# Optimization experiments

Measured on AMD Instinct MI355X. Metric: run time of the kernel, lower is better.

## Reference

```python
import jax, jax.numpy as jnp
import numpy as np

B, S, DM = 4, 8192, 1024
N_RED = 16384   # tokens merged into their right neighbor
N_SAVE = 16384  # tokens kept; must be divisible by B


def setup_inputs() -> dict:
    key = jax.random.key(0)
    k1, k2, k3, k4 = jax.random.split(key, 4)
    x = jax.random.normal(k1, (B, S, DM), dtype=jnp.float32)
    W = jax.random.normal(k2, (DM, DM), dtype=jnp.float32) * (1.0 / np.sqrt(DM))
    ids_to_reduce = jax.random.randint(k3, (N_RED,), 0, B * S - 1, dtype=jnp.int64)
    ids_to_save = jax.random.randint(k4, (N_SAVE,), 0, B * S, dtype=jnp.int64)
    return {"x": x, "W": W, "ids_to_save": ids_to_save, "ids_to_reduce": ids_to_reduce}


def reference(x, W, ids_to_save, ids_to_reduce):
    batch_size, _, dm = x.shape
    xf = x.reshape(-1, dm)                       # [B*S, dm]
    reduced = xf[ids_to_reduce]                  # gather  [N_RED, dm]
    transformed = (reduced @ W.T).astype(jnp.float32)  # Linear, no bias
    xf = xf.at[ids_to_reduce + 1].add(transformed)     # scatter-add into right neighbor
    saved = xf[ids_to_save]                      # gather  [N_SAVE, dm]
    return saved.reshape(batch_size, -1, dm)     # [B, N_SAVE//B, dm]
```

## Files before the change

kernel.cpp:

```cpp
#include <hip/hip_runtime.h>

#define DM    1024
#define NTOK  32768
#define NRED  16384
#define NSAVE 16384

typedef __attribute__((ext_vector_type(8))) short bf16x8;
typedef __attribute__((ext_vector_type(4))) float f32x4;

__device__ __forceinline__ ushort f2bf(float f) {
    union { float f; unsigned u; } v; v.f = f;
    unsigned r = (v.u + 0x7FFF + ((v.u >> 16) & 1)) >> 16;
    return (ushort)r;
}
__device__ __forceinline__ float bf2f(ushort u) {
    union { unsigned u; float f; } v; v.u = ((unsigned)u) << 16;
    return v.f;
}

__global__ __launch_bounds__(256) void init_kernel(int* __restrict__ cnt,
                                                   int* __restrict__ need,
                                                   int* __restrict__ inv,
                                                   int* __restrict__ counter) {
    int t = blockIdx.x * 256 + threadIdx.x;
    if (t < NTOK) { cnt[t] = 0; need[t] = 0; inv[t] = -1; }
    if (t == 0) *counter = 0;
}

__global__ __launch_bounds__(256) void convw_kernel(const float* __restrict__ W,
                                                    ushort* __restrict__ Wb) {
    int i = blockIdx.x * 256 + threadIdx.x;
    float4 v = ((const float4*)W)[i];
    ushort4 o;
    o.x = f2bf(v.x); o.y = f2bf(v.y); o.z = f2bf(v.z); o.w = f2bf(v.w);
    ((ushort4*)Wb)[i] = o;
}

__global__ __launch_bounds__(256) void prep_kernel(const int* __restrict__ red,
                                                   const int* __restrict__ sav,
                                                   int* __restrict__ cnt,
                                                   int* __restrict__ need) {
    int j = blockIdx.x * 256 + threadIdx.x;
    if (j >= NRED) return;
    atomicAdd(&cnt[red[j]], 1);
    int s = sav[j];
    if (s > 0) need[s - 1] = 1;
}

__global__ __launch_bounds__(256) void compact_kernel(const int* __restrict__ cnt,
                                                      const int* __restrict__ need,
                                                      int* __restrict__ inv,
                                                      int* __restrict__ list,
                                                      int* __restrict__ counter) {
    int t = blockIdx.x * 256 + threadIdx.x;
    if (t >= NTOK) return;
    if (need[t] && cnt[t] > 0) {
        int pos = atomicAdd(counter, 1);
        inv[t] = pos;
        list[pos] = t;
    }
}

#define BM 64
#define BN 128
#define BK 32

__global__ __launch_bounds__(256) void gemm_kernel(const float* __restrict__ X,
                                                   const ushort* __restrict__ Wb,
                                                   const int* __restrict__ list,
                                                   const int* __restrict__ counter,
                                                   ushort* __restrict__ Tb) {
    const int M = *counter;
    const int m0 = blockIdx.y * BM;
    if (m0 >= M) return;
    const int n0 = blockIdx.x * BN;

    __shared__ ushort As[BM * BK];
    __shared__ ushort Bs[BN * BK];

    const int tid  = threadIdx.x;
    const int lane = tid & 63;
    const int wid  = tid >> 6;
    const int wr   = wid >> 1;
    const int wc   = wid & 1;
    const int kgrp = lane >> 4;
    const int r16  = lane & 15;

    const int arow  = tid >> 2;
    const int aslot = tid & 3;
    int am = m0 + arow;
    int src = list[am < M ? am : M - 1];
    const float* aptr = X + (size_t)src * DM + aslot * 8;
    const int awidx = arow * BK + ((aslot ^ ((arow >> 1) & 3)) * 8);

    const int brow0 = n0 + (tid >> 2);
    const int bxs   = (tid & 3) ^ ((brow0 >> 1) & 3);
    const ushort* bptr = Wb + (size_t)brow0 * DM + bxs * 8;
    char* BsBase = (char*)Bs + wid * 1024;

    int aoff[2], boff[4];
#pragma unroll
    for (int fm = 0; fm < 2; ++fm) {
        int row = wr * 32 + fm * 16 + r16;
        aoff[fm] = row * BK + ((kgrp ^ ((row >> 1) & 3)) * 8);
    }
#pragma unroll
    for (int fn = 0; fn < 4; ++fn) {
        int row = wc * 64 + fn * 16 + r16;
        boff[fn] = row * BK + ((kgrp ^ ((row >> 1) & 3)) * 8);
    }

    f32x4 acc[2][4] = {};

    for (int k0 = 0; k0 < DM; k0 += BK) {
        float4 a0 = *(const float4*)(aptr + k0);
        float4 a1 = *(const float4*)(aptr + k0 + 4);
        __syncthreads();
        __builtin_amdgcn_global_load_lds(
            (const __attribute__((address_space(1))) unsigned*)(bptr + k0),
            (__attribute__((address_space(3))) unsigned*)(BsBase), 16, 0, 0);
        __builtin_amdgcn_global_load_lds(
            (const __attribute__((address_space(1))) unsigned*)(bptr + k0 + 64 * DM),
            (__attribute__((address_space(3))) unsigned*)(BsBase + 4096), 16, 0, 0);
        bf16x8 av;
        av[0] = (short)f2bf(a0.x); av[1] = (short)f2bf(a0.y);
        av[2] = (short)f2bf(a0.z); av[3] = (short)f2bf(a0.w);
        av[4] = (short)f2bf(a1.x); av[5] = (short)f2bf(a1.y);
        av[6] = (short)f2bf(a1.z); av[7] = (short)f2bf(a1.w);
        *(bf16x8*)(As + awidx) = av;
        __syncthreads();

        bf16x8 af0 = *(const bf16x8*)(As + aoff[0]);
        bf16x8 af1 = *(const bf16x8*)(As + aoff[1]);
        bf16x8 bf0 = *(const bf16x8*)(Bs + boff[0]);
        bf16x8 bf1 = *(const bf16x8*)(Bs + boff[1]);
        bf16x8 bf2 = *(const bf16x8*)(Bs + boff[2]);
        bf16x8 bf3 = *(const bf16x8*)(Bs + boff[3]);
        acc[0][0] = __builtin_amdgcn_mfma_f32_16x16x32_bf16(af0, bf0, acc[0][0], 0, 0, 0);
        acc[0][1] = __builtin_amdgcn_mfma_f32_16x16x32_bf16(af0, bf1, acc[0][1], 0, 0, 0);
        acc[0][2] = __builtin_amdgcn_mfma_f32_16x16x32_bf16(af0, bf2, acc[0][2], 0, 0, 0);
        acc[0][3] = __builtin_amdgcn_mfma_f32_16x16x32_bf16(af0, bf3, acc[0][3], 0, 0, 0);
        acc[1][0] = __builtin_amdgcn_mfma_f32_16x16x32_bf16(af1, bf0, acc[1][0], 0, 0, 0);
        acc[1][1] = __builtin_amdgcn_mfma_f32_16x16x32_bf16(af1, bf1, acc[1][1], 0, 0, 0);
        acc[1][2] = __builtin_amdgcn_mfma_f32_16x16x32_bf16(af1, bf2, acc[1][2], 0, 0, 0);
        acc[1][3] = __builtin_amdgcn_mfma_f32_16x16x32_bf16(af1, bf3, acc[1][3], 0, 0, 0);
    }

#pragma unroll
    for (int fm = 0; fm < 2; ++fm) {
        int mbase = m0 + wr * 32 + fm * 16 + kgrp * 4;
#pragma unroll
        for (int fn = 0; fn < 4; ++fn) {
            int n = n0 + wc * 64 + fn * 16 + r16;
#pragma unroll
            for (int r = 0; r < 4; ++r) {
                int m = mbase + r;
                if (m < M) Tb[(size_t)m * DM + n] = f2bf(acc[fm][fn][r]);
            }
        }
    }
}

__global__ __launch_bounds__(256) void out_kernel(const float* __restrict__ X,
                                                  const ushort* __restrict__ Tb,
                                                  const int* __restrict__ sav,
                                                  const int* __restrict__ cnt,
                                                  const int* __restrict__ inv,
                                                  float* __restrict__ out) {
    int r = blockIdx.x;
    int d = threadIdx.x;
    int s = sav[r];
    const float4* xr = (const float4*)(X + (size_t)s * DM);
    float4 v = xr[d];
    if (s > 0) {
        int t = s - 1;
        int c = cnt[t];
        if (c > 0) {
            float fc = (float)c;
            const ushort4* tr = (const ushort4*)(Tb + (size_t)inv[t] * DM);
            ushort4 w = tr[d];
            v.x += fc * bf2f(w.x); v.y += fc * bf2f(w.y);
            v.z += fc * bf2f(w.z); v.w += fc * bf2f(w.w);
        }
    }
    ((float4*)out)[(size_t)r * (DM / 4) + d] = v;
}

extern "C" void kernel_launch(void* const* d_in, const int* in_sizes, int n_in,
                              void* d_out, int out_size, void* d_ws, size_t ws_size,
                              hipStream_t stream) {
    const float* X   = (const float*)d_in[0];
    const float* W   = (const float*)d_in[1];
    const int*   sav = (const int*)d_in[2];
    const int*   red = (const int*)d_in[3];
    float* out = (float*)d_out;

    char* ws = (char*)d_ws;
    int* counter = (int*)ws;
    int* cnt  = counter + 64;
    int* need = cnt + NTOK;
    int* inv  = need + NTOK;
    int* list = inv + NTOK;
    ushort* Wb = (ushort*)(ws + (1 << 19));
    ushort* Tb = (ushort*)(ws + (4 << 20));

    init_kernel<<<NTOK / 256, 256, 0, stream>>>(cnt, need, inv, counter);
    convw_kernel<<<DM * DM / 4 / 256, 256, 0, stream>>>(W, Wb);
    prep_kernel<<<NRED / 256, 256, 0, stream>>>(red, sav, cnt, need);
    compact_kernel<<<NTOK / 256, 256, 0, stream>>>(cnt, need, inv, list, counter);

    dim3 ggrid(DM / BN, NRED / BM);
    gemm_kernel<<<ggrid, 256, 0, stream>>>(X, Wb, list, counter, Tb);

    out_kernel<<<NSAVE, 256, 0, stream>>>(X, Tb, sav, cnt, inv, out);
}
```

Before: 76.70 us.

## Pre-convert gathered X rows to bf16 and enlarge GEMM tile to 128x128

```diff
diff --git a/kernel.cpp b/kernel.cpp
--- a/kernel.cpp
+++ b/kernel.cpp
@@ -4,6 +4,7 @@
 #define NTOK  32768
 #define NRED  16384
 #define NSAVE 16384
+#define MMAX  16384
 
 typedef __attribute__((ext_vector_type(8))) short bf16x8;
 typedef __attribute__((ext_vector_type(4))) float f32x4;
@@ -18,22 +19,18 @@
     return v.f;
 }
 
-__global__ __launch_bounds__(256) void init_kernel(int* __restrict__ cnt,
-                                                   int* __restrict__ need,
-                                                   int* __restrict__ inv,
-                                                   int* __restrict__ counter) {
+__global__ __launch_bounds__(256) void setup_kernel(const float* __restrict__ W,
+                                                    ushort* __restrict__ Wb,
+                                                    int* __restrict__ cnt,
+                                                    int* __restrict__ need,
+                                                    int* __restrict__ counter) {
     int t = blockIdx.x * 256 + threadIdx.x;
-    if (t < NTOK) { cnt[t] = 0; need[t] = 0; inv[t] = -1; }
-    if (t == 0) *counter = 0;
-}
-
-__global__ __launch_bounds__(256) void convw_kernel(const float* __restrict__ W,
-                                                    ushort* __restrict__ Wb) {
-    int i = blockIdx.x * 256 + threadIdx.x;
-    float4 v = ((const float4*)W)[i];
+    float4 v = ((const float4*)W)[t];
     ushort4 o;
     o.x = f2bf(v.x); o.y = f2bf(v.y); o.z = f2bf(v.z); o.w = f2bf(v.w);
-    ((ushort4*)Wb)[i] = o;
+    ((ushort4*)Wb)[t] = o;
+    if (t < NTOK) { cnt[t] = 0; need[t] = 0; }
+    if (t == 0) *counter = 0;
 }
 
 __global__ __launch_bounds__(256) void prep_kernel(const int* __restrict__ red,
@@ -61,19 +58,32 @@
     }
 }
 
-#define BM 64
+__global__ __launch_bounds__(256) void convx_kernel(const float* __restrict__ X,
+                                                    const int* __restrict__ list,
+                                                    const int* __restrict__ counter,
+                                                    ushort* __restrict__ Xb) {
+    const int M = *counter;
+    for (int r = blockIdx.x; r < M; r += gridDim.x) {
+        int src = list[r];
+        float4 v = ((const float4*)(X + (size_t)src * DM))[threadIdx.x];
+        ushort4 o;
+        o.x = f2bf(v.x); o.y = f2bf(v.y); o.z = f2bf(v.z); o.w = f2bf(v.w);
+        ((ushort4*)(Xb + (size_t)r * DM))[threadIdx.x] = o;
+    }
+}
+
+#define BM 128
 #define BN 128
 #define BK 32
 
-__global__ __launch_bounds__(256) void gemm_kernel(const float* __restrict__ X,
+__global__ __launch_bounds__(256) void gemm_kernel(const ushort* __restrict__ Xb,
                                                    const ushort* __restrict__ Wb,
-                                                   const int* __restrict__ list,
                                                    const int* __restrict__ counter,
                                                    ushort* __restrict__ Tb) {
     const int M = *counter;
-    const int m0 = blockIdx.y * BM;
+    const int m0 = blockIdx.x * BM;
     if (m0 >= M) return;
-    const int n0 = blockIdx.x * BN;
+    const int n0 = blockIdx.y * BN;
 
     __shared__ ushort As[BM * BK];
     __shared__ ushort Bs[BN * BK];
@@ -86,22 +96,21 @@
     const int kgrp = lane >> 4;
     const int r16  = lane & 15;
 
-    const int arow  = tid >> 2;
-    const int aslot = tid & 3;
-    int am = m0 + arow;
-    int src = list[am < M ? am : M - 1];
-    const float* aptr = X + (size_t)src * DM + aslot * 8;
-    const int awidx = arow * BK + ((aslot ^ ((arow >> 1) & 3)) * 8);
-
-    const int brow0 = n0 + (tid >> 2);
-    const int bxs   = (tid & 3) ^ ((brow0 >> 1) & 3);
-    const ushort* bptr = Wb + (size_t)brow0 * DM + bxs * 8;
-    char* BsBase = (char*)Bs + wid * 1024;
-
-    int aoff[2], boff[4];
-#pragma unroll
-    for (int fm = 0; fm < 2; ++fm) {
-        int row = wr * 32 + fm * 16 + r16;
+    const int srow  = tid >> 2;
+    const int sslot = tid & 3;
+    const int sw0 = (sslot ^ ((srow >> 1) & 3)) * 8;
+    const int sw1 = (sslot ^ (((64 + srow) >> 1) & 3)) * 8;
+    const ushort* aptr0 = Xb + (size_t)(m0 + srow) * DM + sw0;
+    const ushort* aptr1 = Xb + (size_t)(m0 + 64 + srow) * DM + sw1;
+    const ushort* bptr0 = Wb + (size_t)(n0 + srow) * DM + sw0;
+    const ushort* bptr1 = Wb + (size_t)(n0 + 64 + srow) * DM + sw1;
+    char* AsD = (char*)As + wid * 1024;
+    char* BsD = (char*)Bs + wid * 1024;
+
+    int aoff[4], boff[4];
+#pragma unroll
+    for (int fm = 0; fm < 4; ++fm) {
+        int row = wr * 64 + fm * 16 + r16;
         aoff[fm] = row * BK + ((kgrp ^ ((row >> 1) & 3)) * 8);
     }
 #pragma unroll
@@ -110,45 +119,39 @@
         boff[fn] = row * BK + ((kgrp ^ ((row >> 1) & 3)) * 8);
     }
 
-    f32x4 acc[2][4] = {};
+    f32x4 acc[4][4] = {};
 
     for (int k0 = 0; k0 < DM; k0 += BK) {
-        float4 a0 = *(const float4*)(aptr + k0);
-        float4 a1 = *(const float4*)(aptr + k0 + 4);
         __syncthreads();
         __builtin_amdgcn_global_load_lds(
-            (const __attribute__((address_space(1))) unsigned*)(bptr + k0),
-            (__attribute__((address_space(3))) unsigned*)(BsBase), 16, 0, 0);
-        __builtin_amdgcn_global_load_lds(
-            (const __attribute__((address_space(1))) unsigned*)(bptr + k0 + 64 * DM),
-            (__attribute__((address_space(3))) unsigned*)(BsBase + 4096), 16, 0, 0);
-        bf16x8 av;
-        av[0] = (short)f2bf(a0.x); av[1] = (short)f2bf(a0.y);
-        av[2] = (short)f2bf(a0.z); av[3] = (short)f2bf(a0.w);
-        av[4] = (short)f2bf(a1.x); av[5] = (short)f2bf(a1.y);
-        av[6] = (short)f2bf(a1.z); av[7] = (short)f2bf(a1.w);
-        *(bf16x8*)(As + awidx) = av;
+            (const __attribute__((address_space(1))) unsigned*)(aptr0 + k0),
+            (__attribute__((address_space(3))) unsigned*)(AsD), 16, 0, 0);
+        __builtin_amdgcn_global_load_lds(
+            (const __attribute__((address_space(1))) unsigned*)(aptr1 + k0),
+            (__attribute__((address_space(3))) unsigned*)(AsD + 4096), 16, 0, 0);
+        __builtin_amdgcn_global_load_lds(
+            (const __attribute__((address_space(1))) unsigned*)(bptr0 + k0),
+            (__attribute__((address_space(3))) unsigned*)(BsD), 16, 0, 0);
+        __builtin_amdgcn_global_load_lds(
+            (const __attribute__((address_space(1))) unsigned*)(bptr1 + k0),
+            (__attribute__((address_space(3))) unsigned*)(BsD + 4096), 16, 0, 0);
         __syncthreads();
 
-        bf16x8 af0 = *(const bf16x8*)(As + aoff[0]);
-        bf16x8 af1 = *(const bf16x8*)(As + aoff[1]);
-        bf16x8 bf0 = *(const bf16x8*)(Bs + boff[0]);
-        bf16x8 bf1 = *(const bf16x8*)(Bs + boff[1]);
-        bf16x8 bf2 = *(const bf16x8*)(Bs + boff[2]);
-        bf16x8 bf3 = *(const bf16x8*)(Bs + boff[3]);
-        acc[0][0] = __builtin_amdgcn_mfma_f32_16x16x32_bf16(af0, bf0, acc[0][0], 0, 0, 0);
-        acc[0][1] = __builtin_amdgcn_mfma_f32_16x16x32_bf16(af0, bf1, acc[0][1], 0, 0, 0);
-        acc[0][2] = __builtin_amdgcn_mfma_f32_16x16x32_bf16(af0, bf2, acc[0][2], 0, 0, 0);
-        acc[0][3] = __builtin_amdgcn_mfma_f32_16x16x32_bf16(af0, bf3, acc[0][3], 0, 0, 0);
-        acc[1][0] = __builtin_amdgcn_mfma_f32_16x16x32_bf16(af1, bf0, acc[1][0], 0, 0, 0);
-        acc[1][1] = __builtin_amdgcn_mfma_f32_16x16x32_bf16(af1, bf1, acc[1][1], 0, 0, 0);
-        acc[1][2] = __builtin_amdgcn_mfma_f32_16x16x32_bf16(af1, bf2, acc[1][2], 0, 0, 0);
-        acc[1][3] = __builtin_amdgcn_mfma_f32_16x16x32_bf16(af1, bf3, acc[1][3], 0, 0, 0);
-    }
-
-#pragma unroll
-    for (int fm = 0; fm < 2; ++fm) {
-        int mbase = m0 + wr * 32 + fm * 16 + kgrp * 4;
+        bf16x8 af[4], bf[4];
+#pragma unroll
+        for (int i = 0; i < 4; ++i) af[i] = *(const bf16x8*)(As + aoff[i]);
+#pragma unroll
+        for (int j = 0; j < 4; ++j) bf[j] = *(const bf16x8*)(Bs + boff[j]);
+#pragma unroll
+        for (int i = 0; i < 4; ++i)
+#pragma unroll
+            for (int j = 0; j < 4; ++j)
+                acc[i][j] = __builtin_amdgcn_mfma_f32_16x16x32_bf16(af[i], bf[j], acc[i][j], 0, 0, 0);
+    }
+
+#pragma unroll
+    for (int fm = 0; fm < 4; ++fm) {
+        int mbase = m0 + wr * 64 + fm * 16 + kgrp * 4;
 #pragma unroll
         for (int fn = 0; fn < 4; ++fn) {
             int n = n0 + wc * 64 + fn * 16 + r16;
@@ -202,15 +205,16 @@
     int* inv  = need + NTOK;
     int* list = inv + NTOK;
     ushort* Wb = (ushort*)(ws + (1 << 19));
-    ushort* Tb = (ushort*)(ws + (4 << 20));
-
-    init_kernel<<<NTOK / 256, 256, 0, stream>>>(cnt, need, inv, counter);
-    convw_kernel<<<DM * DM / 4 / 256, 256, 0, stream>>>(W, Wb);
+    ushort* Xb = (ushort*)(ws + (4 << 20));
+    ushort* Tb = (ushort*)(ws + (36u << 20));
+
+    setup_kernel<<<DM * DM / 4 / 256, 256, 0, stream>>>(W, Wb, cnt, need, counter);
     prep_kernel<<<NRED / 256, 256, 0, stream>>>(red, sav, cnt, need);
     compact_kernel<<<NTOK / 256, 256, 0, stream>>>(cnt, need, inv, list, counter);
-
-    dim3 ggrid(DM / BN, NRED / BM);
-    gemm_kernel<<<ggrid, 256, 0, stream>>>(X, Wb, list, counter, Tb);
+    convx_kernel<<<2048, 256, 0, stream>>>(X, list, counter, Xb);
+
+    dim3 ggrid(MMAX / BM, DM / BN);
+    gemm_kernel<<<ggrid, 256, 0, stream>>>(Xb, Wb, counter, Tb);
 
     out_kernel<<<NSAVE, 256, 0, stream>>>(X, Tb, sav, cnt, inv, out);
 }
```

Result: no change. 76.83 us (+0.2%).
